# Kernel tuning notes

Hardware: AMD Instinct MI355X
Metric: run time of the kernel (lower is better)

## Reference

```python
import jax, jax.numpy as jnp
import numpy as np

HIDDEN = 300
N_NODES = 8192
N_CLAIM = 128
ALPHA = 0.5
TOPK_RATIO = 0.3
NUM_STEPS = 3


def setup_inputs() -> dict:
    key = jax.random.key(0)
    ks = jax.random.split(key, 10)
    H_e = jax.random.normal(ks[0], (N_NODES, HIDDEN), dtype=jnp.float32)
    H_c = jax.random.uniform(ks[1], (N_CLAIM, HIDDEN), dtype=jnp.float32)
    adj_e = jax.random.uniform(ks[2], (N_NODES, N_NODES), dtype=jnp.float32)
    # nn.Linear(hidden_dim, 1, bias=False) weight, stored as [hidden,1]
    W_score1 = jax.random.normal(ks[3], (HIDDEN, 1), dtype=jnp.float32) / np.sqrt(HIDDEN)
    # GGNN (hidden=1) GRU-style parameters, each scalar [1,1]
    Wz = jax.random.normal(ks[4], (1, 1), dtype=jnp.float32)
    Uz = jax.random.normal(ks[5], (1, 1), dtype=jnp.float32)
    Wr = jax.random.normal(ks[6], (1, 1), dtype=jnp.float32)
    Ur = jax.random.normal(ks[7], (1, 1), dtype=jnp.float32)
    Wh = jax.random.normal(ks[8], (1, 1), dtype=jnp.float32)
    Uh = jax.random.normal(ks[9], (1, 1), dtype=jnp.float32)
    return {"H_e": H_e, "H_c": H_c, "adj_e": adj_e, "W_score1": W_score1,
            "Wz": Wz, "Uz": Uz, "Wr": Wr, "Ur": Ur, "Wh": Wh, "Uh": Uh}


def _ggnn(h, adj, Wz, Uz, Wr, Ur, Wh, Uh):
    # Standard gated graph NN (Li et al.): message = adj @ h, GRU update. hidden=1.
    def step(h, _):
        a = adj @ h                               # [N,1] aggregated messages
        z = jax.nn.sigmoid(a @ Wz + h @ Uz)
        r = jax.nn.sigmoid(a @ Wr + h @ Ur)
        h_tilde = jnp.tanh(a @ Wh + (r * h) @ Uh)
        h_new = (1.0 - z) * h + z * h_tilde
        return h_new, None
    h_out, _ = jax.lax.scan(step, h, None, length=NUM_STEPS)
    return h_out


def reference(H_e, H_c, adj_e, W_score1, Wz, Uz, Wr, Ur, Wh, Uh):
    n = H_e.shape[0]
    # (11) self-redundancy
    score1 = H_e @ W_score1                       # [N,1]
    # (12) claim-relevance redundancy
    W = jax.nn.softmax(H_e @ H_c.T, axis=-1)      # [N, C]
    weighted_claim = W @ H_c                      # [N, hidden]
    relevance_sum = jnp.sum(weighted_claim, axis=-1, keepdims=True)
    score2 = -jnp.log(relevance_sum + 1e-10)
    # (13) combine
    score = ALPHA * score1 + (1.0 - ALPHA) * score2
    # (14) GGNN refinement over evidence graph
    S = _ggnn(score, adj_e, Wz, Uz, Wr, Ur, Wh, Uh)   # [N,1]
    # prune top-k highest-redundancy nodes (static k)
    k = int(TOPK_RATIO * n)
    order = jnp.argsort(S[:, 0])                  # ascending
    keep_idx = jnp.sort(order[: n - k])           # original node order, like H_e[keep_mask]
    keep_mask = jnp.zeros((n,), dtype=bool).at[keep_idx].set(True)
    H_e_refined = H_e[keep_idx]                   # [N-k, hidden]
    return H_e_refined, keep_mask
```

## Files before the change

kernel.cpp:

```cpp
#include <hip/hip_runtime.h>
#include <math.h>

#define N_NODES 8192
#define N_CLAIM 128
#define HIDDEN  300
#define KEEP    5735
#define KC      50
#define SHCP    132

__global__ __launch_bounds__(512) void score_prep_kernel(
    const float* __restrict__ He, const float* __restrict__ Hc,
    const float* __restrict__ W1, float* __restrict__ score_out) {
  __shared__ float she[32][HIDDEN];
  __shared__ float shc[KC][SHCP];
  const int tid  = threadIdx.x;
  const int wave = tid >> 6, lane = tid & 63;
  const int nb   = blockIdx.x * 32;

  {
    const float4* src4 = (const float4*)(He + (size_t)nb * HIDDEN);
    float4* dst4 = (float4*)&she[0][0];
    for (int i = tid; i < 32 * HIDDEN / 4; i += 512) dst4[i] = src4[i];
  }

  float a[4][2] = {{0.f,0.f},{0.f,0.f},{0.f,0.f},{0.f,0.f}};
  float sA = 0.f, sB = 0.f;
  for (int k0 = 0; k0 < HIDDEN; k0 += KC) {
    __syncthreads();
    for (int idx = tid; idx < N_CLAIM * (KC / 2); idx += 512) {
      int j  = idx / (KC / 2);
      int kk = idx - j * (KC / 2);
      float2 v = *(const float2*)(Hc + j * HIDDEN + k0 + 2 * kk);
      shc[2 * kk][j]     = v.x;
      shc[2 * kk + 1][j] = v.y;
    }
    __syncthreads();
    #pragma unroll 5
    for (int k = 0; k < KC; k += 2) {
      float2 ca = ((const float2*)&shc[k][0])[lane];
      float2 cb = ((const float2*)&shc[k + 1][0])[lane];
      sA += ca.x + cb.x;
      sB += ca.y + cb.y;
      #pragma unroll
      for (int n = 0; n < 4; ++n) {
        float2 h2v = ((const float2*)&she[wave * 4 + n][0])[(k0 + k) >> 1];
        a[n][0] = fmaf(h2v.x, ca.x, fmaf(h2v.y, cb.x, a[n][0]));
        a[n][1] = fmaf(h2v.x, ca.y, fmaf(h2v.y, cb.y, a[n][1]));
      }
    }
  }

  float res[4];
  #pragma unroll
  for (int n = 0; n < 4; ++n) {
    float m = fmaxf(a[n][0], a[n][1]);
    #pragma unroll
    for (int s = 32; s; s >>= 1) m = fmaxf(m, __shfl_xor(m, s));
    float e0 = expf(a[n][0] - m), e1 = expf(a[n][1] - m);
    float den = e0 + e1, num = e0 * sA + e1 * sB;
    #pragma unroll
    for (int s = 32; s; s >>= 1) { den += __shfl_xor(den, s); num += __shfl_xor(num, s); }
    float s1 = 0.f;
    for (int k = lane; k < HIDDEN; k += 64) s1 = fmaf(she[wave * 4 + n][k], W1[k], s1);
    #pragma unroll
    for (int s = 32; s; s >>= 1) s1 += __shfl_xor(s1, s);
    res[n] = 0.5f * s1 + 0.5f * (-logf(num / den + 1e-10f));
  }
  if (lane == 0) {
    int n0 = nb + wave * 4;
    #pragma unroll
    for (int n = 0; n < 4; ++n) score_out[n0 + n] = res[n];
  }
}

__device__ inline float gru_update(float acc, float hi,
                                   float Wz, float Uz, float Wr, float Ur,
                                   float Wh, float Uh) {
  float z  = 1.f / (1.f + expf(-(acc * Wz + hi * Uz)));
  float r  = 1.f / (1.f + expf(-(acc * Wr + hi * Ur)));
  float ht = tanhf(acc * Wh + (r * hi) * Uh);
  return (1.f - z) * hi + z * ht;
}

__global__ __launch_bounds__(256) void ggnn_step1(
    const float* __restrict__ adj, const float* __restrict__ h_in,
    float* __restrict__ h_out, float* __restrict__ a_out,
    float* __restrict__ rowsum_out,
    const float* __restrict__ pWz, const float* __restrict__ pUz,
    const float* __restrict__ pWr, const float* __restrict__ pUr,
    const float* __restrict__ pWh, const float* __restrict__ pUh) {
  const int wave = threadIdx.x >> 6, lane = threadIdx.x & 63;
  const int row  = blockIdx.x * 4 + wave;
  const float4* __restrict__ a4 = (const float4*)(adj + (size_t)row * N_NODES);
  const float4* __restrict__ h4 = (const float4*)h_in;
  float acc = 0.f, rs = 0.f;
  #pragma unroll 8
  for (int it = 0; it < N_NODES / 256; ++it) {
    float4 a = a4[it * 64 + lane];
    float4 h = h4[it * 64 + lane];
    acc = fmaf(a.x, h.x, acc); acc = fmaf(a.y, h.y, acc);
    acc = fmaf(a.z, h.z, acc); acc = fmaf(a.w, h.w, acc);
    rs += (a.x + a.y) + (a.z + a.w);
  }
  #pragma unroll
  for (int s = 32; s; s >>= 1) { acc += __shfl_xor(acc, s); rs += __shfl_xor(rs, s); }
  if (lane == 0) {
    a_out[row] = acc;
    rowsum_out[row] = rs;
    h_out[row] = gru_update(acc, h_in[row], pWz[0], pUz[0], pWr[0], pUr[0], pWh[0], pUh[0]);
  }
}

__device__ inline unsigned int block_excl_scan_1024(unsigned int v, unsigned int* wsum,
                                                    int wave, int lane, int tid) {
  unsigned int sc = v;
  #pragma unroll
  for (int off = 1; off < 64; off <<= 1) {
    unsigned int o = __shfl_up(sc, off);
    if (lane >= off) sc += o;
  }
  __syncthreads();
  if (lane == 63) wsum[wave] = sc;
  __syncthreads();
  if (tid == 0) {
    unsigned int run = 0;
    for (int w = 0; w < 16; ++w) { unsigned int t = wsum[w]; wsum[w] = run; run += t; }
  }
  __syncthreads();
  return wsum[wave] + sc - v;
}

__device__ inline float block_dot_8192(const float* __restrict__ adjrow,
                                       const float4* __restrict__ h4,
                                       float* wred, int tid, int wave, int lane) {
  const float4* a4 = (const float4*)adjrow;
  float acc = 0.f;
  #pragma unroll
  for (int it = 0; it < 2; ++it) {
    int idx = tid + it * 1024;
    float4 a = a4[idx]; float4 h = h4[idx];
    acc = fmaf(a.x, h.x, fmaf(a.y, h.y, fmaf(a.z, h.z, fmaf(a.w, h.w, acc))));
  }
  #pragma unroll
  for (int s = 32; s; s >>= 1) acc += __shfl_xor(acc, s);
  if (lane == 0) wred[wave] = acc;
  __syncthreads();
  if (tid == 0) { float t = 0.f; for (int w = 0; w < 16; ++w) t += wred[w]; wred[0] = t; }
  __syncthreads();
  float r = wred[0];
  __syncthreads();
  return r;
}

__global__ __launch_bounds__(1024) void fused_refine_select(
    const float* __restrict__ h0, const float* __restrict__ h1,
    const float* __restrict__ a1, const float* __restrict__ rsum,
    const float* __restrict__ adj,
    float* __restrict__ mask_out, int* __restrict__ keep_idx,
    const float* __restrict__ pWz, const float* __restrict__ pUz,
    const float* __restrict__ pWr, const float* __restrict__ pUr,
    const float* __restrict__ pWh, const float* __restrict__ pUh) {
  __shared__ float h2s[N_NODES];
  __shared__ float a2s[N_NODES];
  __shared__ unsigned int keyz[N_NODES];
  __shared__ unsigned int hist[256];
  __shared__ unsigned int rbits[256];
  __shared__ unsigned int wsum[16];
  __shared__ float wred[16];
  __shared__ int s_same, s_eqc, s_nresc;
  __shared__ unsigned int sh_b, sh_newr, sh_prefix, sh_r;

  const int tid = threadIdx.x;
  const int wave = tid >> 6, lane = tid & 63;
  const int base = tid * 8;
  const float Wz = pWz[0], Uz = pUz[0], Wr = pWr[0], Ur = pUr[0];
  const float Wh = pWh[0], Uh = pUh[0];

  if (tid == 0) { s_same = 1; s_eqc = 1; s_nresc = 0; }
  if (tid < 256) rbits[tid] = 0u;
  __syncthreads();
  const float c0 = h1[0];
  {
    const float4* hc4 = (const float4*)h1;
    const float4* hp4 = (const float4*)h0;
    int same = 1, eqc = 1;
    for (int i = tid; i < N_NODES / 4; i += 1024) {
      float4 x = hc4[i], y = hp4[i];
      same &= (x.x == y.x) & (x.y == y.y) & (x.z == y.z) & (x.w == y.w);
      eqc  &= (x.x == c0) & (x.y == c0) & (x.z == c0) & (x.w == c0);
    }
    if (!same) atomicAnd(&s_same, 0);
    if (!eqc)  atomicAnd(&s_eqc, 0);
  }
  __syncthreads();
  {
    const int fsame = s_same, feqc = s_eqc;
    if (fsame) {
      for (int r = base; r < base + 8; ++r) {
        float acc = a1[r];
        a2s[r] = acc;
        h2s[r] = gru_update(acc, h1[r], Wz, Uz, Wr, Ur, Wh, Uh);
      }
    } else if (feqc) {
      for (int r = base; r < base + 8; ++r) {
        float acc = c0 * rsum[r];
        a2s[r] = acc;
        float zarg = acc * Wz + c0 * Uz;
        float wt   = acc * Wh;
        if (zarg <= -200.f) { h2s[r] = c0; }
        else if (zarg >= 200.f && fabsf(wt) - fabsf(c0 * Uh) >= 30.f) {
          h2s[r] = copysignf(1.f, wt);
        } else {
          atomicOr(&rbits[r >> 5], 1u << (r & 31)); atomicAdd(&s_nresc, 1);
        }
      }
    } else {
      for (int r = base; r < base + 8; ++r) atomicOr(&rbits[r >> 5], 1u << (r & 31));
      if (tid == 0) atomicAdd(&s_nresc, N_NODES);
    }
  }
  __syncthreads();
  if (s_nresc > 0) {
    for (int w = 0; w < 256; ++w) {
      unsigned int bits = rbits[w];
      while (bits) {
        int b = __ffs(bits) - 1; bits &= bits - 1;
        int i = w * 32 + b;
        float acc = block_dot_8192(adj + (size_t)i * N_NODES, (const float4*)h1,
                                   wred, tid, wave, lane);
        if (tid == 0) { a2s[i] = acc; h2s[i] = gru_update(acc, h1[i], Wz, Uz, Wr, Ur, Wh, Uh); }
      }
    }
  }
  __syncthreads();

  if (tid == 0) { s_same = 1; s_eqc = 1; s_nresc = 0; }
  if (tid < 256) rbits[tid] = 0u;
  __syncthreads();
  const float c1 = h2s[0];
  {
    const float4* hc4 = (const float4*)h2s;
    const float4* hp4 = (const float4*)h1;
    int same = 1, eqc = 1;
    for (int i = tid; i < N_NODES / 4; i += 1024) {
      float4 x = hc4[i], y = hp4[i];
      same &= (x.x == y.x) & (x.y == y.y) & (x.z == y.z) & (x.w == y.w);
      eqc  &= (x.x == c1) & (x.y == c1) & (x.z == c1) & (x.w == c1);
    }
    if (!same) atomicAnd(&s_same, 0);
    if (!eqc)  atomicAnd(&s_eqc, 0);
  }
  __syncthreads();
  {
    const int fsame = s_same, feqc = s_eqc;
    if (fsame) {
      for (int r = base; r < base + 8; ++r) {
        float acc = a2s[r];
        keyz[r] = __float_as_uint(gru_update(acc, h2s[r], Wz, Uz, Wr, Ur, Wh, Uh));
      }
    } else if (feqc) {
      for (int r = base; r < base + 8; ++r) {
        float acc = c1 * rsum[r];
        float zarg = acc * Wz + c1 * Uz;
        float wt   = acc * Wh;
        if (zarg <= -200.f) { keyz[r] = __float_as_uint(c1); }
        else if (zarg >= 200.f && fabsf(wt) - fabsf(c1 * Uh) >= 30.f) {
          keyz[r] = __float_as_uint(copysignf(1.f, wt));
        } else {
          atomicOr(&rbits[r >> 5], 1u << (r & 31)); atomicAdd(&s_nresc, 1);
        }
      }
    } else {
      for (int r = base; r < base + 8; ++r) atomicOr(&rbits[r >> 5], 1u << (r & 31));
      if (tid == 0) atomicAdd(&s_nresc, N_NODES);
    }
  }
  __syncthreads();
  if (s_nresc > 0) {
    for (int w = 0; w < 256; ++w) {
      unsigned int bits = rbits[w];
      while (bits) {
        int b = __ffs(bits) - 1; bits &= bits - 1;
        int i = w * 32 + b;
        float acc = block_dot_8192(adj + (size_t)i * N_NODES, (const float4*)h2s,
                                   wred, tid, wave, lane);
        if (tid == 0)
          keyz[i] = __float_as_uint(gru_update(acc, h2s[i], Wz, Uz, Wr, Ur, Wh, Uh));
      }
    }
  }
  __syncthreads();

  for (int i = tid; i < N_NODES; i += 1024) {
    unsigned int u = keyz[i];
    keyz[i] = (u & 0x80000000u) ? ~u : (u | 0x80000000u);
  }
  if (tid == 0) { sh_prefix = 0u; sh_r = KEEP; }
  __syncthreads();

  for (int pass = 0; pass < 4; ++pass) {
    const int shift = 24 - pass * 8;
    if (tid < 256) hist[tid] = 0u;
    __syncthreads();
    const unsigned int pref = sh_prefix;
    const unsigned int r    = sh_r;
    #pragma unroll
    for (int i = 0; i < 8; ++i) {
      unsigned int k = keyz[base + i];
      bool match = (pass == 0) || ((k >> (shift + 8)) == pref);
      unsigned int d = match ? ((k >> shift) & 255u) : 256u;
      unsigned long long m = ~0ull;
      #pragma unroll
      for (int b = 0; b < 9; ++b) {
        unsigned long long bal = __ballot((d >> b) & 1u);
        m &= ((d >> b) & 1u) ? bal : ~bal;
      }
      int leader = __ffsll((unsigned long long)m) - 1;
      if (lane == leader && d < 256u)
        atomicAdd(&hist[d], (unsigned int)__popcll(m));
    }
    __syncthreads();
    if (wave == 0) {
      unsigned int t0 = hist[lane * 4], t1 = hist[lane * 4 + 1];
      unsigned int t2 = hist[lane * 4 + 2], t3 = hist[lane * 4 + 3];
      unsigned int tot = t0 + t1 + t2 + t3;
      unsigned int sc = tot;
      #pragma unroll
      for (int off = 1; off < 64; off <<= 1) {
        unsigned int o = __shfl_up(sc, off);
        if (lane >= off) sc += o;
      }
      unsigned int e = sc - tot;
      unsigned int p0 = e + t0, p1 = p0 + t1, p2 = p1 + t2, p3 = p2 + t3;
      if (r > e  && r <= p0) { sh_b = lane * 4;     sh_newr = r - e;  }
      if (r > p0 && r <= p1) { sh_b = lane * 4 + 1; sh_newr = r - p0; }
      if (r > p1 && r <= p2) { sh_b = lane * 4 + 2; sh_newr = r - p1; }
      if (r > p2 && r <= p3) { sh_b = lane * 4 + 3; sh_newr = r - p2; }
    }
    __syncthreads();
    if (tid == 0) { sh_prefix = (pref << 8) | sh_b; sh_r = sh_newr; }
    __syncthreads();
  }
  const unsigned int Kk = sh_prefix;
  const unsigned int tk = sh_r;

  unsigned int eqc = 0;
  #pragma unroll
  for (int i = 0; i < 8; ++i) eqc += (keyz[base + i] == Kk) ? 1u : 0u;
  const unsigned int eqbase = block_excl_scan_1024(eqc, wsum, wave, lane, tid);

  unsigned int runeq = eqbase, kc = 0;
  #pragma unroll
  for (int i = 0; i < 8; ++i) {
    unsigned int k = keyz[base + i];
    bool kp;
    if (k == Kk) { kp = (runeq < tk); ++runeq; } else kp = (k < Kk);
    kc += kp ? 1u : 0u;
  }
  unsigned int pos = block_excl_scan_1024(kc, wsum, wave, lane, tid);

  runeq = eqbase;
  #pragma unroll
  for (int i = 0; i < 8; ++i) {
    unsigned int k = keyz[base + i];
    bool kp;
    if (k == Kk) { kp = (runeq < tk); ++runeq; } else kp = (k < Kk);
    mask_out[base + i] = kp ? 1.0f : 0.0f;
    if (kp) keep_idx[pos++] = base + i;
  }
}

__global__ __launch_bounds__(256) void gather_kernel(
    const float* __restrict__ He, const int* __restrict__ keep_idx,
    float* __restrict__ out) {
  int t = blockIdx.x * 256 + threadIdx.x;
  if (t >= KEEP * (HIDDEN / 4)) return;
  int p = t / (HIDDEN / 4);
  int c = t - p * (HIDDEN / 4);
  const float4* src = (const float4*)(He + (size_t)keep_idx[p] * HIDDEN);
  ((float4*)out)[t] = src[c];
}

extern "C" void kernel_launch(void* const* d_in, const int* in_sizes, int n_in,
                              void* d_out, int out_size, void* d_ws, size_t ws_size,
                              hipStream_t stream) {
  const float* He  = (const float*)d_in[0];
  const float* Hc  = (const float*)d_in[1];
  const float* adj = (const float*)d_in[2];
  const float* W1  = (const float*)d_in[3];
  const float* Wz  = (const float*)d_in[4];
  const float* Uz  = (const float*)d_in[5];
  const float* Wr  = (const float*)d_in[6];
  const float* Ur  = (const float*)d_in[7];
  const float* Wh  = (const float*)d_in[8];
  const float* Uh  = (const float*)d_in[9];
  float* out = (float*)d_out;

  float* ws   = (float*)d_ws;
  float* h0   = ws;
  float* h1   = ws + 1 * N_NODES;
  float* a1   = ws + 2 * N_NODES;
  float* rsum = ws + 3 * N_NODES;
  int* keep_idx = (int*)(ws + 4 * N_NODES);

  float* mask_out = out + (size_t)KEEP * HIDDEN;

  score_prep_kernel  <<<N_NODES / 32, 512, 0, stream>>>(He, Hc, W1, h0);
  ggnn_step1         <<<N_NODES / 4, 256, 0, stream>>>(adj, h0, h1, a1, rsum,
                                                       Wz, Uz, Wr, Ur, Wh, Uh);
  fused_refine_select<<<1, 1024, 0, stream>>>(h0, h1, a1, rsum, adj, mask_out, keep_idx,
                                              Wz, Uz, Wr, Ur, Wh, Uh);
  gather_kernel      <<<(KEEP * (HIDDEN / 4) + 255) / 256, 256, 0, stream>>>(He, keep_idx, out);
}
```

Measured before the change: 127.7 us.

## Restructure GGNN step1 so 1024-thread blocks cover 16 rows and reuse h

Each 1024-thread block now processes 16 adjacency rows one at a time, with the whole block cooperating on each row. The h vector slice is loaded into registers once per block and reused across the 16 rows. The next row is prefetched into registers while the current one is reduced. This removes redundant h loads and gives more loads in flight per row, but adds two block-wide barriers per row and serialises the row loop, which could limit memory-level parallelism on the 256 MB adjacency stream.

```diff
diff --git a/kernel.cpp b/kernel.cpp
--- a/kernel.cpp
+++ b/kernel.cpp
@@ -82,32 +82,62 @@
   return (1.f - z) * hi + z * ht;
 }
 
-__global__ __launch_bounds__(256) void ggnn_step1(
+__global__ __launch_bounds__(1024, 8) void ggnn_step1(
     const float* __restrict__ adj, const float* __restrict__ h_in,
     float* __restrict__ h_out, float* __restrict__ a_out,
     float* __restrict__ rowsum_out,
     const float* __restrict__ pWz, const float* __restrict__ pUz,
     const float* __restrict__ pWr, const float* __restrict__ pUr,
     const float* __restrict__ pWh, const float* __restrict__ pUh) {
-  const int wave = threadIdx.x >> 6, lane = threadIdx.x & 63;
-  const int row  = blockIdx.x * 4 + wave;
-  const float4* __restrict__ a4 = (const float4*)(adj + (size_t)row * N_NODES);
+  __shared__ float s_wa[16], s_wq[16];
+  __shared__ float s_a[16], s_rs[16];
+  const int tid  = threadIdx.x;
+  const int wave = tid >> 6, lane = tid & 63;
+  const int rbase = blockIdx.x * 16;
+
   const float4* __restrict__ h4 = (const float4*)h_in;
-  float acc = 0.f, rs = 0.f;
-  #pragma unroll 8
-  for (int it = 0; it < N_NODES / 256; ++it) {
-    float4 a = a4[it * 64 + lane];
-    float4 h = h4[it * 64 + lane];
-    acc = fmaf(a.x, h.x, acc); acc = fmaf(a.y, h.y, acc);
-    acc = fmaf(a.z, h.z, acc); acc = fmaf(a.w, h.w, acc);
-    rs += (a.x + a.y) + (a.z + a.w);
-  }
-  #pragma unroll
-  for (int s = 32; s; s >>= 1) { acc += __shfl_xor(acc, s); rs += __shfl_xor(rs, s); }
-  if (lane == 0) {
+  const float4 hA = h4[tid];
+  const float4 hB = h4[tid + 1024];
+
+  const float4* __restrict__ arow = (const float4*)(adj + (size_t)rbase * N_NODES);
+  float4 aA = arow[tid];
+  float4 aB = arow[tid + 1024];
+
+  #pragma unroll 1
+  for (int r = 0; r < 16; ++r) {
+    float4 nA = aA, nB = aB;
+    if (r < 15) {
+      const float4* nrow = arow + (size_t)(r + 1) * (N_NODES / 4);
+      nA = nrow[tid];
+      nB = nrow[tid + 1024];
+    }
+    float p = aA.x * hA.x;
+    p = fmaf(aA.y, hA.y, p); p = fmaf(aA.z, hA.z, p); p = fmaf(aA.w, hA.w, p);
+    p = fmaf(aB.x, hB.x, p); p = fmaf(aB.y, hB.y, p);
+    p = fmaf(aB.z, hB.z, p); p = fmaf(aB.w, hB.w, p);
+    float q = (aA.x + aA.y) + (aA.z + aA.w) + (aB.x + aB.y) + (aB.z + aB.w);
+    #pragma unroll
+    for (int s = 32; s; s >>= 1) { p += __shfl_xor(p, s); q += __shfl_xor(q, s); }
+    if (lane == 0) { s_wa[wave] = p; s_wq[wave] = q; }
+    __syncthreads();
+    if (wave == 0) {
+      float pa = (lane < 16) ? s_wa[lane] : 0.f;
+      float qa = (lane < 16) ? s_wq[lane] : 0.f;
+      #pragma unroll
+      for (int s = 8; s; s >>= 1) { pa += __shfl_xor(pa, s); qa += __shfl_xor(qa, s); }
+      if (lane == 0) { s_a[r] = pa; s_rs[r] = qa; }
+    }
+    __syncthreads();
+    aA = nA; aB = nB;
+  }
+
+  if (wave == 0 && lane < 16) {
+    const int row = rbase + lane;
+    const float acc = s_a[lane], rs = s_rs[lane];
     a_out[row] = acc;
     rowsum_out[row] = rs;
-    h_out[row] = gru_update(acc, h_in[row], pWz[0], pUz[0], pWr[0], pUr[0], pWh[0], pUh[0]);
+    h_out[row] = gru_update(acc, h_in[row],
+                            pWz[0], pUz[0], pWr[0], pUr[0], pWh[0], pUh[0]);
   }
 }
 
@@ -406,8 +436,8 @@
   float* mask_out = out + (size_t)KEEP * HIDDEN;
 
   score_prep_kernel  <<<N_NODES / 32, 512, 0, stream>>>(He, Hc, W1, h0);
-  ggnn_step1         <<<N_NODES / 4, 256, 0, stream>>>(adj, h0, h1, a1, rsum,
-                                                       Wz, Uz, Wr, Ur, Wh, Uh);
+  ggnn_step1         <<<N_NODES / 16, 1024, 0, stream>>>(adj, h0, h1, a1, rsum,
+                                                         Wz, Uz, Wr, Ur, Wh, Uh);
   fused_refine_select<<<1, 1024, 0, stream>>>(h0, h1, a1, rsum, adj, mask_out, keep_idx,
                                               Wz, Uz, Wr, Ur, Wh, Uh);
   gather_kernel      <<<(KEEP * (HIDDEN / 4) + 255) / 256, 256, 0, stream>>>(He, keep_idx, out);
```

Measured after the change: 126.6 us. About the same (-0.9%).
